# Kernel optimization log

Hardware: AMD Instinct MI355X
Metric: run time of the kernel (lower is better)

Reference implementation:

```python
import jax, jax.numpy as jnp
import numpy as np

N_NODES = 50000
N_EDGES = 800000
IN_DIM = 256
HIDDEN = 64
HEADS1 = 4
HEADS2 = 1
N_CLASSES = 64
NEG_SLOPE = 0.2


def setup_inputs() -> dict:
    key = jax.random.key(0)
    ks = jax.random.split(key, 12)
    x = jax.random.normal(ks[0], (N_NODES, IN_DIM), dtype=jnp.float32)
    src = jax.random.randint(ks[1], (N_EDGES,), 0, N_NODES, dtype=jnp.int32)
    dst = jax.random.randint(ks[2], (N_EDGES,), 0, N_NODES, dtype=jnp.int32)
    s1 = 1.0 / np.sqrt(IN_DIM)
    s2 = 1.0 / np.sqrt(HIDDEN * HEADS1)
    W1 = jax.random.normal(ks[3], (IN_DIM, HEADS1 * HIDDEN), dtype=jnp.float32) * s1
    aL1 = jax.random.normal(ks[4], (HEADS1, HIDDEN), dtype=jnp.float32) * 0.1
    aR1 = jax.random.normal(ks[5], (HEADS1, HIDDEN), dtype=jnp.float32) * 0.1
    b1 = jnp.zeros((HEADS1 * HIDDEN,), dtype=jnp.float32)
    W2 = jax.random.normal(ks[6], (HEADS1 * HIDDEN, HEADS2 * N_CLASSES), dtype=jnp.float32) * s2
    aL2 = jax.random.normal(ks[7], (HEADS2, N_CLASSES), dtype=jnp.float32) * 0.1
    aR2 = jax.random.normal(ks[8], (HEADS2, N_CLASSES), dtype=jnp.float32) * 0.1
    b2 = jnp.zeros((HEADS2 * N_CLASSES,), dtype=jnp.float32)
    resW2 = jax.random.normal(ks[9], (HEADS1 * HIDDEN, HEADS2 * N_CLASSES), dtype=jnp.float32) * s2
    return {"x": x, "W1": W1, "aL1": aL1, "aR1": aR1, "b1": b1,
            "W2": W2, "aL2": aL2, "aR2": aR2, "b2": b2, "resW2": resW2,
            "src": src, "dst": dst}


def _gat_layer(h, W, aL, aR, b, src, dst, heads, out_dim, res_W=None, activation=None):
    n = h.shape[0]
    feat = (h @ W).reshape(n, heads, out_dim)          # [N, H, D]
    el = jnp.sum(feat * aL, axis=-1)                    # [N, H]
    er = jnp.sum(feat * aR, axis=-1)                    # [N, H]
    e = el[src] + er[dst]                               # [E, H]
    e = jnp.where(e > 0, e, NEG_SLOPE * e)              # leaky_relu
    # edge softmax over incoming edges of each destination node
    m = jax.ops.segment_max(e, dst, num_segments=n)
    ex = jnp.exp(e - m[dst])
    s = jax.ops.segment_sum(ex, dst, num_segments=n)
    sd = s[dst]
    a = ex / jnp.where(sd > 0, sd, 1.0)                 # [E, H]
    msg = feat[src] * a[:, :, None]                     # [E, H, D]
    rst = jax.ops.segment_sum(msg, dst, num_segments=n)  # [N, H, D]
    if res_W is not None:
        rst = rst + (h @ res_W).reshape(n, heads, out_dim)
    rst = rst + b.reshape(1, heads, out_dim)
    if activation is not None:
        rst = activation(rst)
    return rst


def reference(x, W1, aL1, aR1, b1, W2, aL2, aR2, b2, resW2, src, dst):
    h = _gat_layer(x, W1, aL1, aR1, b1, src, dst, HEADS1, HIDDEN,
                   res_W=None, activation=jax.nn.elu)
    h = h.reshape(N_NODES, HEADS1 * HIDDEN)             # flatten(1)
    h = _gat_layer(h, W2, aL2, aR2, b2, src, dst, HEADS2, N_CLASSES,
                   res_W=resW2, activation=None)
    return h.mean(axis=1)                               # mean over heads
```

## Files before the change

kernel.cpp:

```cpp
#include <hip/hip_runtime.h>
#include <hip/hip_bf16.h>
#include <math.h>

#define N_NODES 50000
#define N_EDGES 800000
#define IN_DIM  256
#define HID     64
#define H1      4
#define F1      256
#define NC      64
#define CHUNK   128
#define NB_SCAN 49
#define GEMM1_BLOCKS 800
#define FILL_BLOCKS  ((N_EDGES+255)/256)
#define HIST4_BLOCKS ((N_EDGES/4+255)/256)

typedef __attribute__((ext_vector_type(8))) short short8v;
typedef __attribute__((ext_vector_type(4))) float float4v;

__device__ __forceinline__ float bf2f(unsigned short u){
  union { unsigned int i; float f; } c; c.i = ((unsigned int)u) << 16; return c.f;
}


__global__ __launch_bounds__(256) void hist_prepw_kernel(
    const int* __restrict__ dst, int* __restrict__ counts,
    const float* __restrict__ W1, const float* __restrict__ W2,
    const float* __restrict__ resW2,
    __hip_bfloat16* __restrict__ W1T, __hip_bfloat16* __restrict__ B2T){
  int b = blockIdx.x;
  if (b < HIST4_BLOCKS){
    int e4 = b*256 + threadIdx.x;
    if (e4 < N_EDGES/4){
      int4 d = ((const int4*)dst)[e4];
      atomicAdd(&counts[d.x], 1);
      atomicAdd(&counts[d.y], 1);
      atomicAdd(&counts[d.z], 1);
      atomicAdd(&counts[d.w], 1);
    }
  } else {
    int i = (b - HIST4_BLOCKS)*256 + threadIdx.x;
    if (i < 256*256){
      int n = i >> 8, k = i & 255;
      W1T[n*256 + k] = __float2bfloat16(W1[k*256 + n]);
    } else if (i < 256*256 + 128*256){
      int j = i - 256*256;
      int n = j >> 8, k = j & 255;
      float v = (n < 64) ? W2[k*64 + n] : resW2[k*64 + (n - 64)];
      B2T[n*256 + k] = __float2bfloat16(v);
    }
  }
}


__global__ __launch_bounds__(1024) void scan1_kernel(const int* __restrict__ counts,
                                                     int* __restrict__ part,
                                                     int* __restrict__ bsum, int n){
  __shared__ int wsum[16];
  int b = blockIdx.x, tid = threadIdx.x;
  int i = b*1024 + tid;
  int lane = tid & 63, wid = tid >> 6;
  int x = (i < n) ? counts[i] : 0;
  #pragma unroll
  for (int off = 1; off < 64; off <<= 1){ int t = __shfl_up(x, off); if (lane >= off) x += t; }
  if (lane == 63) wsum[wid] = x;
  __syncthreads();
  if (wid == 0 && lane < 16){
    int w = wsum[lane];
    #pragma unroll
    for (int off = 1; off < 16; off <<= 1){ int t = __shfl_up(w, off); if (lane >= off) w += t; }
    wsum[lane] = w;
  }
  __syncthreads();
  int incl = x + (wid ? wsum[wid-1] : 0);
  if (i < n) part[i] = incl;
  if (tid == 1023) bsum[b] = incl;
}

__global__ __launch_bounds__(1024) void scan3_kernel(const int* __restrict__ part,
                                                     const int* __restrict__ bsum,
                                                     int* __restrict__ row_ptr,
                                                     int* __restrict__ cursor, int n){
  __shared__ int off_s;
  int b = blockIdx.x, tid = threadIdx.x;
  if (tid < 64){
    int orig = (tid < NB_SCAN) ? bsum[tid] : 0;
    int x = orig;
    #pragma unroll
    for (int o = 1; o < 64; o <<= 1){ int t = __shfl_up(x, o); if (tid >= o) x += t; }
    if (tid == b) off_s = x - orig;
  }
  __syncthreads();
  int i = b*1024 + tid;
  if (i < n){
    int v = part[i] + off_s;
    row_ptr[i+1] = v; cursor[i+1] = v;
  }
  if (i == 0){ row_ptr[0] = 0; cursor[0] = 0; }
}


template<int LAYER, bool AFP32>
__device__ __forceinline__ void gemm_body(
    const void* __restrict__ Araw,
    const __hip_bfloat16* __restrict__ BT,
    __hip_bfloat16* __restrict__ Fb,
    float* __restrict__ Res,
    float* __restrict__ el, float* __restrict__ er,
    const float* __restrict__ aL, const float* __restrict__ aR,
    int M, int bm, int bn)
{
  constexpr int K = 256;
  __shared__ __hip_bfloat16 As[128*72];
  __shared__ __hip_bfloat16 Bs[128*72];
  int tid = threadIdx.x;
  int lane = tid & 63, w = tid >> 6;
  int wr = w >> 1, wc = w & 1;
  int l15 = lane & 15, l4 = lane >> 4;

  float4v acc[4][4];
  #pragma unroll
  for (int i=0;i<4;i++)
    #pragma unroll
    for (int j=0;j<4;j++) acc[i][j] = (float4v){0.f,0.f,0.f,0.f};

  for (int kt = 0; kt < K; kt += 64){
    #pragma unroll
    for (int it = 0; it < 4; it++){
      int chunk = tid + it*256;
      int r = chunk >> 3, kc = (chunk & 7)*8;
      int arow = bm*128 + r;
      if (AFP32){
        const float* Af = (const float*)Araw;
        float4 v0 = make_float4(0,0,0,0), v1 = make_float4(0,0,0,0);
        if (arow < M){
          v0 = *(const float4*)&Af[(size_t)arow*K + kt + kc];
          v1 = *(const float4*)&Af[(size_t)arow*K + kt + kc + 4];
        }
        __hip_bfloat16 t[8] = {__float2bfloat16(v0.x),__float2bfloat16(v0.y),
                               __float2bfloat16(v0.z),__float2bfloat16(v0.w),
                               __float2bfloat16(v1.x),__float2bfloat16(v1.y),
                               __float2bfloat16(v1.z),__float2bfloat16(v1.w)};
        *(int4*)&As[r*72 + kc] = *(int4*)t;
      } else {
        const __hip_bfloat16* Ab = (const __hip_bfloat16*)Araw;
        int4 va = make_int4(0,0,0,0);
        if (arow < M) va = *(const int4*)&Ab[(size_t)arow*K + kt + kc];
        *(int4*)&As[r*72 + kc] = va;
      }
      int brow = bn*128 + r;
      int4 vb = *(const int4*)&BT[(size_t)brow*K + kt + kc];
      *(int4*)&Bs[r*72 + kc] = vb;
    }
    __syncthreads();
    short8v af[4][2], bfr[4][2];
    #pragma unroll
    for (int mi=0;mi<4;mi++)
      #pragma unroll
      for (int kf=0;kf<2;kf++)
        af[mi][kf] = *(const short8v*)&As[(wr*64 + mi*16 + l15)*72 + kf*32 + l4*8];
    #pragma unroll
    for (int ni=0;ni<4;ni++)
      #pragma unroll
      for (int kf=0;kf<2;kf++)
        bfr[ni][kf] = *(const short8v*)&Bs[(wc*64 + ni*16 + l15)*72 + kf*32 + l4*8];
    #pragma unroll
    for (int mi=0;mi<4;mi++)
      #pragma unroll
      for (int ni=0;ni<4;ni++){
        acc[mi][ni] = __builtin_amdgcn_mfma_f32_16x16x32_bf16(af[mi][0], bfr[ni][0], acc[mi][ni], 0,0,0);
        acc[mi][ni] = __builtin_amdgcn_mfma_f32_16x16x32_bf16(af[mi][1], bfr[ni][1], acc[mi][ni], 0,0,0);
      }
    __syncthreads();
  }

  if (LAYER == 1){
    int h = bn*2 + wc;
    float aLv[4], aRv[4];
    #pragma unroll
    for (int ni=0;ni<4;ni++){ aLv[ni] = aL[h*64 + ni*16 + l15]; aRv[ni] = aR[h*64 + ni*16 + l15]; }
    #pragma unroll
    for (int mi=0;mi<4;mi++){
      #pragma unroll
      for (int r=0;r<4;r++){
        int row = bm*128 + wr*64 + mi*16 + l4*4 + r;
        float sl = 0.f, sr = 0.f;
        #pragma unroll
        for (int ni=0;ni<4;ni++){ float v = acc[mi][ni][r]; sl += v*aLv[ni]; sr += v*aRv[ni]; }
        #pragma unroll
        for (int off=1; off<16; off<<=1){ sl += __shfl_xor(sl, off); sr += __shfl_xor(sr, off); }
        if (row < M){
          #pragma unroll
          for (int ni=0;ni<4;ni++)
            Fb[(size_t)row*256 + h*64 + ni*16 + l15] = __float2bfloat16(acc[mi][ni][r]);
          if (l15 == 0){ el[row*4 + h] = sl; er[row*4 + h] = sr; }
        }
      }
    }
  } else {
    if (wc == 0){
      float aLv[4], aRv[4];
      #pragma unroll
      for (int ni=0;ni<4;ni++){ aLv[ni] = aL[ni*16 + l15]; aRv[ni] = aR[ni*16 + l15]; }
      #pragma unroll
      for (int mi=0;mi<4;mi++){
        #pragma unroll
        for (int r=0;r<4;r++){
          int row = bm*128 + wr*64 + mi*16 + l4*4 + r;
          float sl = 0.f, sr = 0.f;
          #pragma unroll
          for (int ni=0;ni<4;ni++){ float v = acc[mi][ni][r]; sl += v*aLv[ni]; sr += v*aRv[ni]; }
          #pragma unroll
          for (int off=1; off<16; off<<=1){ sl += __shfl_xor(sl, off); sr += __shfl_xor(sr, off); }
          if (row < M){
            #pragma unroll
            for (int ni=0;ni<4;ni++)
              Fb[(size_t)row*64 + ni*16 + l15] = __float2bfloat16(acc[mi][ni][r]);
            if (l15 == 0){ el[row] = sl; er[row] = sr; }
          }
        }
      }
    } else {
      #pragma unroll
      for (int mi=0;mi<4;mi++){
        #pragma unroll
        for (int r=0;r<4;r++){
          int row = bm*128 + wr*64 + mi*16 + l4*4 + r;
          if (row < M){
            #pragma unroll
            for (int ni=0;ni<4;ni++)
              Res[(size_t)row*64 + ni*16 + l15] = acc[mi][ni][r];
          }
        }
      }
    }
  }
}

__global__ __launch_bounds__(256) void gemm1_fill_kernel(
    const float* __restrict__ x, const __hip_bfloat16* __restrict__ W1T,
    __hip_bfloat16* __restrict__ featb,
    float* __restrict__ el, float* __restrict__ er,
    const float* __restrict__ aL, const float* __restrict__ aR,
    const int* __restrict__ src, const int* __restrict__ dst,
    int* __restrict__ cursor, int* __restrict__ csr_src)
{
  int id = blockIdx.x;
  if (id < GEMM1_BLOCKS){
    int bn = (id >> 3) & 1;
    int bm = (id & 7) | ((id >> 4) << 3);
    if (bm*128 >= N_NODES) return;
    gemm_body<1,true>(x, W1T, featb, nullptr, el, er, aL, aR, N_NODES, bm, bn);
  } else {
    int e = (id - GEMM1_BLOCKS)*256 + threadIdx.x;
    if (e < N_EDGES){
      int slot = atomicAdd(&cursor[dst[e]], 1);
      csr_src[slot] = src[e];
    }
  }
}

__global__ __launch_bounds__(256) void gemm2_kernel(
    const __hip_bfloat16* __restrict__ A, const __hip_bfloat16* __restrict__ BT,
    __hip_bfloat16* __restrict__ Fb, float* __restrict__ Res,
    float* __restrict__ el, float* __restrict__ er,
    const float* __restrict__ aL, const float* __restrict__ aR, int M)
{
  gemm_body<2,false>(A, BT, Fb, Res, el, er, aL, aR, M, blockIdx.x, 0);
}


__global__ __launch_bounds__(256) void agg1_kernel(const int* __restrict__ row_ptr,
                                                   const int* __restrict__ csr_src,
                                                   const float* __restrict__ el,
                                                   const float* __restrict__ er,
                                                   const __hip_bfloat16* __restrict__ featb,
                                                   const float* __restrict__ bias,
                                                   __hip_bfloat16* __restrict__ h1b, int N){
  __shared__ int   ssh[4][CHUNK];
  __shared__ float wsh[4][CHUNK][4];
  int lane = threadIdx.x & 63, wv = threadIdx.x >> 6;
  int n = blockIdx.x*4 + wv;
  if (n >= N) return;
  int rs = row_ptr[n], re = row_ptr[n+1];
  int half = lane >> 5;
  int l31 = lane & 31;
  int hl = l31 >> 3;
  float4 ern4 = *(const float4*)&er[(size_t)n*4];
  float ernv[4] = {ern4.x, ern4.y, ern4.z, ern4.w};
  float acc[8] = {0.f,0.f,0.f,0.f,0.f,0.f,0.f,0.f};
  float ssum4[4] = {0.f,0.f,0.f,0.f};

  for (int base = rs; base < re; base += CHUNK){
    int cnt = min(CHUNK, re - base);
    int padded = (cnt + 7) & ~7;
    for (int t = lane; t < padded; t += 64){
      float w4[4] = {0.f,0.f,0.f,0.f};
      int s = 0;
      if (t < cnt){
        s = csr_src[base + t];
        float4 e4 = *(const float4*)&el[(size_t)s*4];
        float ev[4] = {e4.x, e4.y, e4.z, e4.w};
        #pragma unroll
        for (int h = 0; h < 4; h++){
          float e = ev[h] + ernv[h];
          e = e > 0.f ? e : 0.2f*e;
          float ex = __expf(e);
          w4[h] = ex;
          ssum4[h] += ex;
        }
      }
      ssh[wv][t] = s;
      *(float4*)&wsh[wv][t][0] = make_float4(w4[0], w4[1], w4[2], w4[3]);
    }
    for (int jb = 0; jb < padded; jb += 8){
      int t0 = jb + half, t1 = jb + 2 + half, t2 = jb + 4 + half, t3 = jb + 6 + half;
      int s0 = ssh[wv][t0], s1 = ssh[wv][t1], s2 = ssh[wv][t2], s3 = ssh[wv][t3];
      float w0 = wsh[wv][t0][hl], w1 = wsh[wv][t1][hl];
      float w2 = wsh[wv][t2][hl], w3 = wsh[wv][t3][hl];
      short8v f0 = *(const short8v*)&featb[(size_t)s0*256 + l31*8];
      short8v f1 = *(const short8v*)&featb[(size_t)s1*256 + l31*8];
      short8v f2 = *(const short8v*)&featb[(size_t)s2*256 + l31*8];
      short8v f3 = *(const short8v*)&featb[(size_t)s3*256 + l31*8];
      #pragma unroll
      for (int q = 0; q < 8; q++){
        acc[q] += w0 * bf2f((unsigned short)f0[q]);
        acc[q] += w1 * bf2f((unsigned short)f1[q]);
        acc[q] += w2 * bf2f((unsigned short)f2[q]);
        acc[q] += w3 * bf2f((unsigned short)f3[q]);
      }
    }
  }
  #pragma unroll
  for (int off = 32; off; off >>= 1)
    #pragma unroll
    for (int h = 0; h < 4; h++) ssum4[h] += __shfl_xor(ssum4[h], off);
  #pragma unroll
  for (int q = 0; q < 8; q++) acc[q] += __shfl_xor(acc[q], 32);
  float inv = ssum4[hl] > 0.f ? 1.f/ssum4[hl] : 0.f;
  if (lane < 32){
    float4 b0 = *(const float4*)&bias[l31*8];
    float4 b1v = *(const float4*)&bias[l31*8 + 4];
    float bb[8] = {b0.x,b0.y,b0.z,b0.w,b1v.x,b1v.y,b1v.z,b1v.w};
    __hip_bfloat16 o[8];
    #pragma unroll
    for (int q = 0; q < 8; q++){
      float v = acc[q]*inv + bb[q];
      v = v > 0.f ? v : __expf(v) - 1.f;
      o[q] = __float2bfloat16(v);
    }
    *(short8v*)&h1b[(size_t)n*256 + l31*8] = *(short8v*)o;
  }
}

__global__ __launch_bounds__(256) void agg2_kernel(const int* __restrict__ row_ptr,
                                                   const int* __restrict__ csr_src,
                                                   const float* __restrict__ el,
                                                   const float* __restrict__ er,
                                                   const __hip_bfloat16* __restrict__ f2b,
                                                   const float* __restrict__ res,
                                                   const float* __restrict__ bias,
                                                   float* __restrict__ out, int N){
  __shared__ int   ssh[4][CHUNK];
  __shared__ float wsh[4][CHUNK];
  int lane = threadIdx.x & 63, wv = threadIdx.x >> 6;
  int n = blockIdx.x*4 + wv;
  if (n >= N) return;
  int rs = row_ptr[n], re = row_ptr[n+1];
  int q4 = lane >> 4;
  int l15 = lane & 15;
  float ern = er[n];
  float acc[4] = {0.f,0.f,0.f,0.f};
  float ssum = 0.f;

  for (int base = rs; base < re; base += CHUNK){
    int cnt = min(CHUNK, re - base);
    int padded = (cnt + 15) & ~15;
    for (int t = lane; t < padded; t += 64){
      float w = 0.f; int s = 0;
      if (t < cnt){
        s = csr_src[base + t];
        float e = el[s] + ern;
        e = e > 0.f ? e : 0.2f*e;
        w = __expf(e);
        ssum += w;
      }
      ssh[wv][t] = s;
      wsh[wv][t] = w;
    }
    for (int jb = 0; jb < padded; jb += 16){
      int t0 = jb + q4, t1 = jb + 4 + q4, t2 = jb + 8 + q4, t3 = jb + 12 + q4;
      int s0 = ssh[wv][t0], s1 = ssh[wv][t1], s2 = ssh[wv][t2], s3 = ssh[wv][t3];
      float w0 = wsh[wv][t0], w1 = wsh[wv][t1], w2 = wsh[wv][t2], w3 = wsh[wv][t3];
      ushort4 f0 = *(const ushort4*)&f2b[(size_t)s0*NC + l15*4];
      ushort4 f1 = *(const ushort4*)&f2b[(size_t)s1*NC + l15*4];
      ushort4 f2 = *(const ushort4*)&f2b[(size_t)s2*NC + l15*4];
      ushort4 f3 = *(const ushort4*)&f2b[(size_t)s3*NC + l15*4];
      acc[0] += w0*bf2f(f0.x) + w1*bf2f(f1.x) + w2*bf2f(f2.x) + w3*bf2f(f3.x);
      acc[1] += w0*bf2f(f0.y) + w1*bf2f(f1.y) + w2*bf2f(f2.y) + w3*bf2f(f3.y);
      acc[2] += w0*bf2f(f0.z) + w1*bf2f(f1.z) + w2*bf2f(f2.z) + w3*bf2f(f3.z);
      acc[3] += w0*bf2f(f0.w) + w1*bf2f(f1.w) + w2*bf2f(f2.w) + w3*bf2f(f3.w);
    }
  }
  #pragma unroll
  for (int off = 32; off; off >>= 1) ssum += __shfl_xor(ssum, off);
  #pragma unroll
  for (int q = 0; q < 4; q++){
    acc[q] += __shfl_xor(acc[q], 16);
    acc[q] += __shfl_xor(acc[q], 32);
  }
  float inv = ssum > 0.f ? 1.f/ssum : 0.f;
  if (lane < 16){
    float4 r4 = *(const float4*)&res[(size_t)n*NC + l15*4];
    float4 b4 = *(const float4*)&bias[l15*4];
    float4 o;
    o.x = acc[0]*inv + r4.x + b4.x;
    o.y = acc[1]*inv + r4.y + b4.y;
    o.z = acc[2]*inv + r4.z + b4.z;
    o.w = acc[3]*inv + r4.w + b4.w;
    *(float4*)&out[(size_t)n*NC + l15*4] = o;
  }
}


extern "C" void kernel_launch(void* const* d_in, const int* in_sizes, int n_in,
                              void* d_out, int out_size, void* d_ws, size_t ws_size,
                              hipStream_t stream){
  const float* x     = (const float*)d_in[0];
  const float* W1    = (const float*)d_in[1];
  const float* aL1   = (const float*)d_in[2];
  const float* aR1   = (const float*)d_in[3];
  const float* b1    = (const float*)d_in[4];
  const float* W2    = (const float*)d_in[5];
  const float* aL2   = (const float*)d_in[6];
  const float* aR2   = (const float*)d_in[7];
  const float* b2    = (const float*)d_in[8];
  const float* resW2 = (const float*)d_in[9];
  const int*   src   = (const int*)d_in[10];
  const int*   dst   = (const int*)d_in[11];
  float* out = (float*)d_out;

  char* p = (char*)d_ws;
  auto alloc = [&](size_t bytes)->void*{
    void* r = (void*)p; p += (bytes + 255) & ~(size_t)255; return r;
  };
  __hip_bfloat16* featb = (__hip_bfloat16*)alloc((size_t)N_NODES*F1*2);
  __hip_bfloat16* h1b   = (__hip_bfloat16*)alloc((size_t)N_NODES*F1*2);
  __hip_bfloat16* f2b   = (__hip_bfloat16*)alloc((size_t)N_NODES*NC*2);
  float* res   = (float*)alloc((size_t)N_NODES*NC*4);
  float* el1   = (float*)alloc((size_t)N_NODES*H1*4);
  float* er1   = (float*)alloc((size_t)N_NODES*H1*4);
  float* el2   = (float*)alloc((size_t)N_NODES*4);
  float* er2   = (float*)alloc((size_t)N_NODES*4);
  int* counts  = (int*)alloc((size_t)N_NODES*4);
  int* part    = (int*)alloc((size_t)N_NODES*4);
  int* bsum    = (int*)alloc((size_t)64*4);
  int* row_ptr = (int*)alloc((size_t)(N_NODES+1)*4);
  int* cursor  = (int*)alloc((size_t)(N_NODES+1)*4);
  int* csr_src = (int*)alloc((size_t)N_EDGES*4);
  __hip_bfloat16* W1T = (__hip_bfloat16*)alloc((size_t)256*256*2);
  __hip_bfloat16* B2T = (__hip_bfloat16*)alloc((size_t)128*256*2);

  int nb = (N_NODES + 1023)/1024;
  int prepw_blocks = (256*256 + 128*256 + 255)/256;
  hipMemsetAsync(counts, 0, (size_t)N_NODES*4, stream);
  hist_prepw_kernel<<<HIST4_BLOCKS + prepw_blocks, 256, 0, stream>>>(dst, counts,
                                                                     W1, W2, resW2, W1T, B2T);
  scan1_kernel<<<nb, 1024, 0, stream>>>(counts, part, bsum, N_NODES);
  scan3_kernel<<<nb, 1024, 0, stream>>>(part, bsum, row_ptr, cursor, N_NODES);

  gemm1_fill_kernel<<<GEMM1_BLOCKS + FILL_BLOCKS, 256, 0, stream>>>(
      x, W1T, featb, el1, er1, aL1, aR1, src, dst, cursor, csr_src);

  agg1_kernel<<<(N_NODES+3)/4, 256, 0, stream>>>(row_ptr, csr_src, el1, er1, featb, b1, h1b, N_NODES);

  gemm2_kernel<<<(N_NODES+127)/128, 256, 0, stream>>>(h1b, B2T, f2b, res,
                                                      el2, er2, aL2, aR2, N_NODES);
  agg2_kernel<<<(N_NODES+3)/4, 256, 0, stream>>>(row_ptr, csr_src, el2, er2, f2b, res, b2, out, N_NODES);
}
```

Baseline: 210.3 us.

## Transpose MFMA operands for vectorized epilogue stores; split agg1 feature columns across blocks

The GEMM epilogue swaps the A and B operands of the MFMA so that each lane holds four consecutive output columns of one row. This allows packed bf16 and float4 stores, and the el/er attention reductions drop from four shuffles to two. agg1 now splits the 256 feature columns into two 128-column halves handled by separate blocks, which doubles the grid and halves per-thread accumulator state. The cost is that the edge-weight computation (exp over el) is duplicated across the two column halves, and each gather is narrower.

```diff
diff --git a/kernel.cpp b/kernel.cpp
--- a/kernel.cpp
+++ b/kernel.cpp
@@ -168,68 +168,91 @@
     for (int mi=0;mi<4;mi++)
       #pragma unroll
       for (int ni=0;ni<4;ni++){
-        acc[mi][ni] = __builtin_amdgcn_mfma_f32_16x16x32_bf16(af[mi][0], bfr[ni][0], acc[mi][ni], 0,0,0);
-        acc[mi][ni] = __builtin_amdgcn_mfma_f32_16x16x32_bf16(af[mi][1], bfr[ni][1], acc[mi][ni], 0,0,0);
+        acc[mi][ni] = __builtin_amdgcn_mfma_f32_16x16x32_bf16(bfr[ni][0], af[mi][0], acc[mi][ni], 0,0,0);
+        acc[mi][ni] = __builtin_amdgcn_mfma_f32_16x16x32_bf16(bfr[ni][1], af[mi][1], acc[mi][ni], 0,0,0);
       }
     __syncthreads();
   }
 
   if (LAYER == 1){
     int h = bn*2 + wc;
-    float aLv[4], aRv[4];
-    #pragma unroll
-    for (int ni=0;ni<4;ni++){ aLv[ni] = aL[h*64 + ni*16 + l15]; aRv[ni] = aR[h*64 + ni*16 + l15]; }
+    float aLv[4][4], aRv[4][4];
+    #pragma unroll
+    for (int ni=0;ni<4;ni++){
+      float4 a = *(const float4*)&aL[h*64 + ni*16 + l4*4];
+      float4 bvv = *(const float4*)&aR[h*64 + ni*16 + l4*4];
+      aLv[ni][0]=a.x; aLv[ni][1]=a.y; aLv[ni][2]=a.z; aLv[ni][3]=a.w;
+      aRv[ni][0]=bvv.x; aRv[ni][1]=bvv.y; aRv[ni][2]=bvv.z; aRv[ni][3]=bvv.w;
+    }
     #pragma unroll
     for (int mi=0;mi<4;mi++){
-      #pragma unroll
-      for (int r=0;r<4;r++){
-        int row = bm*128 + wr*64 + mi*16 + l4*4 + r;
+      int row = bm*128 + wr*64 + mi*16 + l15;
+      float sl = 0.f, sr = 0.f;
+      ushort4 packs[4];
+      #pragma unroll
+      for (int ni=0;ni<4;ni++){
+        __hip_bfloat16 o[4];
+        #pragma unroll
+        for (int r=0;r<4;r++){
+          float v = acc[mi][ni][r];
+          sl += v*aLv[ni][r]; sr += v*aRv[ni][r];
+          o[r] = __float2bfloat16(v);
+        }
+        packs[ni] = *(ushort4*)o;
+      }
+      if (row < M){
+        #pragma unroll
+        for (int ni=0;ni<4;ni++)
+          *(ushort4*)&Fb[(size_t)row*256 + h*64 + ni*16 + l4*4] = packs[ni];
+      }
+      sl += __shfl_xor(sl, 16); sl += __shfl_xor(sl, 32);
+      sr += __shfl_xor(sr, 16); sr += __shfl_xor(sr, 32);
+      if (l4 == 0 && row < M){ el[row*4 + h] = sl; er[row*4 + h] = sr; }
+    }
+  } else {
+    if (wc == 0){
+      float aLv[4][4], aRv[4][4];
+      #pragma unroll
+      for (int ni=0;ni<4;ni++){
+        float4 a = *(const float4*)&aL[ni*16 + l4*4];
+        float4 bvv = *(const float4*)&aR[ni*16 + l4*4];
+        aLv[ni][0]=a.x; aLv[ni][1]=a.y; aLv[ni][2]=a.z; aLv[ni][3]=a.w;
+        aRv[ni][0]=bvv.x; aRv[ni][1]=bvv.y; aRv[ni][2]=bvv.z; aRv[ni][3]=bvv.w;
+      }
+      #pragma unroll
+      for (int mi=0;mi<4;mi++){
+        int row = bm*128 + wr*64 + mi*16 + l15;
         float sl = 0.f, sr = 0.f;
+        ushort4 packs[4];
         #pragma unroll
-        for (int ni=0;ni<4;ni++){ float v = acc[mi][ni][r]; sl += v*aLv[ni]; sr += v*aRv[ni]; }
-        #pragma unroll
-        for (int off=1; off<16; off<<=1){ sl += __shfl_xor(sl, off); sr += __shfl_xor(sr, off); }
+        for (int ni=0;ni<4;ni++){
+          __hip_bfloat16 o[4];
+          #pragma unroll
+          for (int r=0;r<4;r++){
+            float v = acc[mi][ni][r];
+            sl += v*aLv[ni][r]; sr += v*aRv[ni][r];
+            o[r] = __float2bfloat16(v);
+          }
+          packs[ni] = *(ushort4*)o;
+        }
         if (row < M){
           #pragma unroll
           for (int ni=0;ni<4;ni++)
-            Fb[(size_t)row*256 + h*64 + ni*16 + l15] = __float2bfloat16(acc[mi][ni][r]);
-          if (l15 == 0){ el[row*4 + h] = sl; er[row*4 + h] = sr; }
+            *(ushort4*)&Fb[(size_t)row*64 + ni*16 + l4*4] = packs[ni];
         }
-      }
-    }
-  } else {
-    if (wc == 0){
-      float aLv[4], aRv[4];
-      #pragma unroll
-      for (int ni=0;ni<4;ni++){ aLv[ni] = aL[ni*16 + l15]; aRv[ni] = aR[ni*16 + l15]; }
+        sl += __shfl_xor(sl, 16); sl += __shfl_xor(sl, 32);
+        sr += __shfl_xor(sr, 16); sr += __shfl_xor(sr, 32);
+        if (l4 == 0 && row < M){ el[row] = sl; er[row] = sr; }
+      }
+    } else {
       #pragma unroll
       for (int mi=0;mi<4;mi++){
-        #pragma unroll
-        for (int r=0;r<4;r++){
-          int row = bm*128 + wr*64 + mi*16 + l4*4 + r;
-          float sl = 0.f, sr = 0.f;
+        int row = bm*128 + wr*64 + mi*16 + l15;
+        if (row < M){
           #pragma unroll
-          for (int ni=0;ni<4;ni++){ float v = acc[mi][ni][r]; sl += v*aLv[ni]; sr += v*aRv[ni]; }
-          #pragma unroll
-          for (int off=1; off<16; off<<=1){ sl += __shfl_xor(sl, off); sr += __shfl_xor(sr, off); }
-          if (row < M){
-            #pragma unroll
-            for (int ni=0;ni<4;ni++)
-              Fb[(size_t)row*64 + ni*16 + l15] = __float2bfloat16(acc[mi][ni][r]);
-            if (l15 == 0){ el[row] = sl; er[row] = sr; }
-          }
-        }
-      }
-    } else {
-      #pragma unroll
-      for (int mi=0;mi<4;mi++){
-        #pragma unroll
-        for (int r=0;r<4;r++){
-          int row = bm*128 + wr*64 + mi*16 + l4*4 + r;
-          if (row < M){
-            #pragma unroll
-            for (int ni=0;ni<4;ni++)
-              Res[(size_t)row*64 + ni*16 + l15] = acc[mi][ni][r];
+          for (int ni=0;ni<4;ni++){
+            float4 o = make_float4(acc[mi][ni][0], acc[mi][ni][1], acc[mi][ni][2], acc[mi][ni][3]);
+            *(float4*)&Res[(size_t)row*64 + ni*16 + l4*4] = o;
           }
         }
       }
@@ -279,16 +302,19 @@
                                                    __hip_bfloat16* __restrict__ h1b, int N){
   __shared__ int   ssh[4][CHUNK];
   __shared__ float wsh[4][CHUNK][4];
+  int b = blockIdx.x;
+  int slot = b & 7, ch = slot >> 2, sub = slot & 3, g = b >> 3;
   int lane = threadIdx.x & 63, wv = threadIdx.x >> 6;
-  int n = blockIdx.x*4 + wv;
+  int n = g*16 + sub*4 + wv;
   if (n >= N) return;
   int rs = row_ptr[n], re = row_ptr[n+1];
   int half = lane >> 5;
   int l31 = lane & 31;
-  int hl = l31 >> 3;
+  int c0 = ch*128 + l31*4;
+  int hl = c0 >> 6;
   float4 ern4 = *(const float4*)&er[(size_t)n*4];
   float ernv[4] = {ern4.x, ern4.y, ern4.z, ern4.w};
-  float acc[8] = {0.f,0.f,0.f,0.f,0.f,0.f,0.f,0.f};
+  float acc[4] = {0.f,0.f,0.f,0.f};
   float ssum4[4] = {0.f,0.f,0.f,0.f};
 
   for (int base = rs; base < re; base += CHUNK){
@@ -318,17 +344,14 @@
       int s0 = ssh[wv][t0], s1 = ssh[wv][t1], s2 = ssh[wv][t2], s3 = ssh[wv][t3];
       float w0 = wsh[wv][t0][hl], w1 = wsh[wv][t1][hl];
       float w2 = wsh[wv][t2][hl], w3 = wsh[wv][t3][hl];
-      short8v f0 = *(const short8v*)&featb[(size_t)s0*256 + l31*8];
-      short8v f1 = *(const short8v*)&featb[(size_t)s1*256 + l31*8];
-      short8v f2 = *(const short8v*)&featb[(size_t)s2*256 + l31*8];
-      short8v f3 = *(const short8v*)&featb[(size_t)s3*256 + l31*8];
-      #pragma unroll
-      for (int q = 0; q < 8; q++){
-        acc[q] += w0 * bf2f((unsigned short)f0[q]);
-        acc[q] += w1 * bf2f((unsigned short)f1[q]);
-        acc[q] += w2 * bf2f((unsigned short)f2[q]);
-        acc[q] += w3 * bf2f((unsigned short)f3[q]);
-      }
+      ushort4 f0 = *(const ushort4*)&featb[(size_t)s0*256 + c0];
+      ushort4 f1 = *(const ushort4*)&featb[(size_t)s1*256 + c0];
+      ushort4 f2 = *(const ushort4*)&featb[(size_t)s2*256 + c0];
+      ushort4 f3 = *(const ushort4*)&featb[(size_t)s3*256 + c0];
+      acc[0] += w0*bf2f(f0.x) + w1*bf2f(f1.x) + w2*bf2f(f2.x) + w3*bf2f(f3.x);
+      acc[1] += w0*bf2f(f0.y) + w1*bf2f(f1.y) + w2*bf2f(f2.y) + w3*bf2f(f3.y);
+      acc[2] += w0*bf2f(f0.z) + w1*bf2f(f1.z) + w2*bf2f(f2.z) + w3*bf2f(f3.z);
+      acc[3] += w0*bf2f(f0.w) + w1*bf2f(f1.w) + w2*bf2f(f2.w) + w3*bf2f(f3.w);
     }
   }
   #pragma unroll
@@ -336,20 +359,19 @@
     #pragma unroll
     for (int h = 0; h < 4; h++) ssum4[h] += __shfl_xor(ssum4[h], off);
   #pragma unroll
-  for (int q = 0; q < 8; q++) acc[q] += __shfl_xor(acc[q], 32);
+  for (int q = 0; q < 4; q++) acc[q] += __shfl_xor(acc[q], 32);
   float inv = ssum4[hl] > 0.f ? 1.f/ssum4[hl] : 0.f;
   if (lane < 32){
-    float4 b0 = *(const float4*)&bias[l31*8];
-    float4 b1v = *(const float4*)&bias[l31*8 + 4];
-    float bb[8] = {b0.x,b0.y,b0.z,b0.w,b1v.x,b1v.y,b1v.z,b1v.w};
-    __hip_bfloat16 o[8];
-    #pragma unroll
-    for (int q = 0; q < 8; q++){
+    float4 b4 = *(const float4*)&bias[c0];
+    float bb[4] = {b4.x, b4.y, b4.z, b4.w};
+    __hip_bfloat16 o[4];
+    #pragma unroll
+    for (int q = 0; q < 4; q++){
       float v = acc[q]*inv + bb[q];
       v = v > 0.f ? v : __expf(v) - 1.f;
       o[q] = __float2bfloat16(v);
     }
-    *(short8v*)&h1b[(size_t)n*256 + l31*8] = *(short8v*)o;
+    *(ushort4*)&h1b[(size_t)n*256 + c0] = *(ushort4*)o;
   }
 }
 
@@ -472,7 +494,7 @@
   gemm1_fill_kernel<<<GEMM1_BLOCKS + FILL_BLOCKS, 256, 0, stream>>>(
       x, W1T, featb, el1, er1, aL1, aR1, src, dst, cursor, csr_src);
 
-  agg1_kernel<<<(N_NODES+3)/4, 256, 0, stream>>>(row_ptr, csr_src, el1, er1, featb, b1, h1b, N_NODES);
+  agg1_kernel<<<25000, 256, 0, stream>>>(row_ptr, csr_src, el1, er1, featb, b1, h1b, N_NODES);
 
   gemm2_kernel<<<(N_NODES+127)/128, 256, 0, stream>>>(h1b, B2T, f2b, res,
                                                       el2, er2, aL2, aR2, N_NODES);
```

After: 212.7 us. No clear change (+1.1%).
